# Performance work log

Hardware: AMD Instinct MI355X
Metric: run time of the kernel (lower is better)

Reference implementation:

```python
import jax, jax.numpy as jnp
import numpy as np

NUM_HEADS = 8  # config.num_heads


def setup_inputs() -> dict:
    key = jax.random.key(0)
    k0, k1, k2, k3, k4 = jax.random.split(key, 5)
    B, N, C, E = 32, 20000, 8, 512
    query_embeddings = jax.random.normal(k0, (B, E), dtype=jnp.float32)
    all_embeddings = jax.random.normal(k1, (N, E), dtype=jnp.float32)
    label_mask = jax.random.bernoulli(k2, 0.5, (N, C))  # bool multi-label mask
    # per-class MultiheadAttention q/k in-projection params (torch Linear convention: x @ W.T + b)
    Wq = jax.random.normal(k3, (C, E, E), dtype=jnp.float32) * 0.02
    Wk = jax.random.normal(k4, (C, E, E), dtype=jnp.float32) * 0.02
    bq = jnp.zeros((C, E), dtype=jnp.float32)
    bk = jnp.zeros((C, E), dtype=jnp.float32)
    return {
        "query_embeddings": query_embeddings,
        "all_embeddings": all_embeddings,
        "label_mask": label_mask,
        "Wq": Wq,
        "bq": bq,
        "Wk": Wk,
        "bk": bk,
        "n_samples": 5,
    }


def reference(query_embeddings, all_embeddings, label_mask, Wq, bq, Wk, bk, n_samples):
    """Vectorized-over-classes version of EmbeddingSelector.get_similar_samples.

    For each class c: q = query @ Wq[c].T + bq[c]; k_c over the class's database
    members; per-head scaled-dot softmax; attn weights averaged over heads
    (torch MHA need_weights default); top-k over class members. Non-members are
    masked to -inf before softmax, so they get weight 0 and (since every class
    has >> n_samples members) never enter the top-k -- identical math to the
    per-class gather loop, with global indices returned directly.
    """
    C, E, _ = Wq.shape
    H = NUM_HEADS
    dh = E // H
    B = query_embeddings.shape[0]
    N = all_embeddings.shape[0]

    # per-class projections (torch Linear: x @ W.T + b)
    q = jnp.einsum('be,cfe->cbf', query_embeddings, Wq) + bq[:, None, :]   # (C,B,E)
    k = jnp.einsum('ne,cfe->cnf', all_embeddings, Wk) + bk[:, None, :]     # (C,N,E)
    q = q.reshape(C, B, H, dh)
    k = k.reshape(C, N, H, dh)

    scale = 1.0 / jnp.sqrt(jnp.asarray(dh, q.dtype))
    scores = jnp.einsum('cbhd,cnhd->cbhn', q, k) * scale                   # (C,B,H,N)
    member = jnp.transpose(label_mask)[:, None, None, :]                   # (C,1,1,N)
    scores = jnp.where(member, scores, jnp.asarray(-1e9, scores.dtype))
    attn = jax.nn.softmax(scores, axis=-1).mean(axis=2)                    # (C,B,N) head-avg

    weights, indices = jax.lax.top_k(attn, n_samples)                      # (C,B,ns)
    result_weights = jnp.transpose(weights, (1, 0, 2))                     # (B,C,ns)
    result_indices = jnp.transpose(indices, (1, 0, 2)).astype(jnp.int32)   # (B,C,ns) global ids
    return result_indices, result_weights
```

## Files before the change

kernel.cpp:

```cpp
#include <hip/hip_runtime.h>
#include <math.h>

#define B_  32
#define N_  20000
#define C_  8
#define E_  512
#define H_  8
#define SCALE 0.125f
#define UNSC  9.765625e-4f

#define CHUNK 1024
#define NCH   20
#define NC3   157
#define NCG   20
#define SSZ ((size_t)B_ * H_ * N_)

typedef __attribute__((ext_vector_type(8))) _Float16 h8_t;
typedef __attribute__((ext_vector_type(8))) short   s8_t;
typedef __attribute__((ext_vector_type(4))) float f32x4;

#define MFMAH(a, b, c) __builtin_amdgcn_mfma_f32_16x16x32_f16(a, b, c, 0, 0, 0)

#define GLOAD_LDS16(g, l)                                              \
    __builtin_amdgcn_global_load_lds(                                  \
        (const __attribute__((address_space(1))) unsigned int*)(g),    \
        (__attribute__((address_space(3))) unsigned int*)(l), 16, 0, 0)

__device__ inline unsigned short f16_round(float x, float& fv) {
    _Float16 h = (_Float16)x;
    fv = (float)h;
    union { _Float16 hh; unsigned short us; } u;
    u.hh = h;
    return u.us;
}

__global__ __launch_bounds__(256) void k_q2(
        const float* __restrict__ x, const float* __restrict__ Wq,
        const float* __restrict__ bq, float* __restrict__ q) {
    int ft = blockIdx.x, c = blockIdx.y;
    int f0 = ft * 8;
    __shared__ float wsm[8][66];
    __shared__ float xs[32][66];
    int tid = threadIdx.x;
    int b = tid & 31, fs = tid >> 5;
    float acc = 0.f;
    const float* W = Wq + (size_t)c * E_ * E_;
    for (int k0 = 0; k0 < E_; k0 += 64) {
        __syncthreads();
        for (int i = tid; i < 512; i += 256)
            wsm[i >> 6][i & 63] = W[(size_t)(f0 + (i >> 6)) * E_ + k0 + (i & 63)];
        for (int i = tid; i < 2048; i += 256)
            xs[i >> 6][i & 63] = x[(size_t)(i >> 6) * E_ + k0 + (i & 63)];
        __syncthreads();
        #pragma unroll
        for (int kk = 0; kk < 64; ++kk)
            acc += xs[b][kk] * wsm[fs][kk];
    }
    q[((size_t)c * B_ + b) * E_ + f0 + fs] = acc + bq[c * E_ + f0 + fs];
}

__global__ __launch_bounds__(256) void k_u2(
        const float* __restrict__ q, const float* __restrict__ Wk,
        const float* __restrict__ bk, float* __restrict__ u,
        float* __restrict__ qb) {
    int et = blockIdx.x, h = blockIdx.y, c = blockIdx.z;
    int e0 = et * 64;
    __shared__ float qs[32][66];
    __shared__ float wk[64][66];
    int tid = threadIdx.x;
    int b = tid & 31, es = tid >> 5;
    for (int i = tid; i < 2048; i += 256)
        qs[i >> 6][i & 63] = q[((size_t)c * B_ + (i >> 6)) * E_ + h * 64 + (i & 63)];
    const float* W = Wk + (size_t)c * E_ * E_ + (size_t)(h * 64) * E_;
    for (int i = tid; i < 4096; i += 256)
        wk[i >> 6][i & 63] = W[(size_t)(i >> 6) * E_ + e0 + (i & 63)];
    __syncthreads();
    float acc[8] = {};
    for (int d = 0; d < 64; ++d) {
        float qv = qs[b][d];
        #pragma unroll
        for (int j = 0; j < 8; ++j)
            acc[j] += qv * wk[d][es * 8 + j];
    }
    float* urow = u + ((size_t)c * 256 + b * 8 + h) * E_ + e0 + es * 8;
    #pragma unroll
    for (int j = 0; j < 8; ++j) urow[j] = acc[j];
    if (et == 0 && es == 0) {
        float s = 0.f;
        const float* bkr = bk + c * E_ + h * 64;
        for (int d = 0; d < 64; ++d) s += qs[b][d] * bkr[d];
        qb[c * 256 + b * 8 + h] = s;
    }
}

#define U2P ((size_t)C_ * 16 * 16 * 512)

__global__ void k_split_u2(const float* __restrict__ u, short* __restrict__ u2) {
    int bx = blockIdx.x;
    int ks = bx & 15, mt = (bx >> 4) & 15, c = bx >> 8;
    int lane = threadIdx.x;
    int m  = mt * 16 + (lane & 15);
    int k0 = ks * 32 + (lane >> 4) * 8;
    const float* up = u + ((size_t)c * 256 + m) * 512 + k0;
    size_t base = ((((size_t)c * 16 + mt) * 16 + ks) * 512) + (size_t)lane * 8;
    s8_t vh, vm;
    #pragma unroll
    for (int j = 0; j < 8; ++j) {
        float x = up[j] * 32.0f, fh, fm;
        vh[j] = (short)f16_round(x, fh);
        vm[j] = (short)f16_round(x - fh, fm);
    }
    *(s8_t*)(u2 + base)       = vh;
    *(s8_t*)(u2 + U2P + base) = vm;
}

__global__ void k_split_A2(const float* __restrict__ A, short* __restrict__ A2t) {
    int nc = blockIdx.x, ks = blockIdx.y;
    int tid = threadIdx.x;
    int n = tid >> 1, kg = (tid & 1) * 2;
    int gn = nc * 128 + n;
    const float* ap = A + (size_t)gn * 512 + ks * 32 + kg * 8;
    s8_t vh[2], vm[2];
    #pragma unroll
    for (int g = 0; g < 2; ++g)
        #pragma unroll
        for (int j = 0; j < 8; ++j) {
            float x = (gn < N_) ? ap[g * 8 + j] * 32.0f : 0.f;
            float fh, fm;
            vh[g][j] = (short)f16_round(x, fh);
            vm[g][j] = (short)f16_round(x - fh, fm);
        }
    short* outp = A2t + ((size_t)nc * 16 + ks) * 8192 + n * 32;
    #pragma unroll
    for (int g = 0; g < 2; ++g) {
        int p = ((kg + g) + (n >> 1)) & 3;
        *(s8_t*)(outp + p * 8)        = vh[g];
        *(s8_t*)(outp + 4096 + p * 8) = vm[g];
    }
}

__global__ __launch_bounds__(256, 2) void k_scores_mfma(
        const short* __restrict__ u2, const short* __restrict__ A2t,
        const float* __restrict__ qb, const int* __restrict__ mask,
        float* __restrict__ S, float* __restrict__ Zpart, int c0, int CB) {
    __shared__ __align__(16) short As[16384];
    __shared__ float sQb[256];
    __shared__ int   sMask[128];
    int bx = blockIdx.x;
    int x    = bx & 7;
    int rest = bx >> 3;
    int z    = rest % CB;
    int g    = rest / CB;
    int nc   = g * 8 + x;
    if (nc >= NC3) return;
    int c  = c0 + z;
    int tid = threadIdx.x;
    int lane = tid & 63, w = tid >> 6;
    int quad = lane >> 4, l15 = lane & 15;
    int n0 = nc * 128;

    sQb[tid] = qb[c * 256 + tid];
    if (tid < 128) {
        int n = n0 + tid;
        sMask[tid] = (n < N_) ? mask[(size_t)n * C_ + c] : 0;
    }

    f32x4 acc[4][8];
    #pragma unroll
    for (int i = 0; i < 4; ++i)
        #pragma unroll
        for (int j = 0; j < 8; ++j)
            acc[i][j] = (f32x4){0.f, 0.f, 0.f, 0.f};

    const char* tb = (const char*)A2t + (size_t)nc * 262144;

    for (int ks2 = 0; ks2 < 8; ++ks2) {
        __syncthreads();
        const char* src = tb + (size_t)ks2 * 32768;
        #pragma unroll
        for (int t = 0; t < 8; ++t) {
            int seg = w * 8 + t;
            GLOAD_LDS16(src + (size_t)seg * 1024 + lane * 16,
                        (char*)As + seg * 1024);
        }
        __syncthreads();

        #pragma unroll
        for (int kh = 0; kh < 2; ++kh) {
            int ks = ks2 * 2 + kh;
            const short* Ab = As + kh * 8192;
            h8_t af[4][2];
            #pragma unroll
            for (int mt = 0; mt < 4; ++mt) {
                size_t ub = ((((size_t)c * 16 + (w * 4 + mt)) * 16 + ks) * 512)
                            + (size_t)lane * 8;
                af[mt][0] = *(const h8_t*)(u2 + ub);
                af[mt][1] = *(const h8_t*)(u2 + U2P + ub);
            }
            #pragma unroll
            for (int nt = 0; nt < 8; ++nt) {
                int r = nt * 16 + l15;
                const short* bp = Ab + r * 32 + ((quad + (r >> 1)) & 3) * 8;
                h8_t b0 = *(const h8_t*)bp;
                h8_t b1 = *(const h8_t*)(bp + 4096);
                #pragma unroll
                for (int mt = 0; mt < 4; ++mt) {
                    f32x4 a = acc[mt][nt];
                    a = MFMAH(af[mt][0], b0, a);
                    a = MFMAH(af[mt][0], b1, a);
                    a = MFMAH(af[mt][1], b0, a);
                    acc[mt][nt] = a;
                }
            }
        }
    }

    float* Sc = S + (size_t)z * SSZ;
    #pragma unroll
    for (int mt = 0; mt < 4; ++mt) {
        float rs[4] = {0.f, 0.f, 0.f, 0.f};
        #pragma unroll
        for (int nt = 0; nt < 8; ++nt) {
            int nl = nt * 16 + l15;
            int n = n0 + nl;
            int mem = sMask[nl];
            #pragma unroll
            for (int r = 0; r < 4; ++r) {
                int m = w * 64 + mt * 16 + quad * 4 + r;
                float sc = SCALE * (acc[mt][nt][r] * UNSC + sQb[m]);
                float ev = mem ? __expf(sc) : 0.f;
                rs[r] += ev;
                if (n < N_) Sc[(size_t)m * N_ + n] = ev;
            }
        }
        #pragma unroll
        for (int r = 0; r < 4; ++r) {
            float v = rs[r];
            v += __shfl_xor(v, 1); v += __shfl_xor(v, 2);
            v += __shfl_xor(v, 4); v += __shfl_xor(v, 8);
            if (l15 == 0) {
                int m = w * 64 + mt * 16 + quad * 4 + r;
                Zpart[((size_t)nc * C_ + c) * 256 + m] = v;
            }
        }
    }
}

__global__ void k_zsum(const float* __restrict__ Zpart, float* __restrict__ Z, int c0) {
    int c = c0 + blockIdx.x;
    int i = c * 256 + threadIdx.x;
    float s = 0.f;
    for (int nc = 0; nc < NC3; ++nc) s += Zpart[(size_t)nc * (C_ * 256) + i];
    Z[i] = s;
}

__global__ __launch_bounds__(256) void k_topk1(
        const float* __restrict__ S, const float* __restrict__ Z,
        float2* __restrict__ cand, int c0, int ns) {
    int chunk = blockIdx.x, b = blockIdx.y, z = blockIdx.z;
    const float* Sc = S + (size_t)z * SSZ;
    int tid = threadIdx.x;
    __shared__ float zr[H_];
    if (tid < H_) zr[tid] = 1.0f / Z[(c0 + z) * (B_ * H_) + b * H_ + tid];
    __syncthreads();
    int n0 = chunk * CHUNK + tid * 4;
    bool valid = n0 < N_;
    float4 a = make_float4(0.f, 0.f, 0.f, 0.f);
    if (valid) {
        #pragma unroll
        for (int h = 0; h < H_; ++h) {
            const float4 sv = *(const float4*)&Sc[(size_t)(b * H_ + h) * N_ + n0];
            float wz = zr[h];
            a.x += sv.x * wz; a.y += sv.y * wz; a.z += sv.z * wz; a.w += sv.w * wz;
        }
    }
    float v[4]; int ix[4];
    v[0] = valid ? a.x * 0.125f : -1.f;
    v[1] = valid ? a.y * 0.125f : -1.f;
    v[2] = valid ? a.z * 0.125f : -1.f;
    v[3] = valid ? a.w * 0.125f : -1.f;
    #pragma unroll
    for (int t = 0; t < 4; ++t) ix[t] = valid ? n0 + t : N_;

    __shared__ float wv[4];
    __shared__ int   wi[4];
    __shared__ int   winS;
    int lane = tid & 63, w = tid >> 6;
    for (int j = 0; j < ns; ++j) {
        float bv = v[0]; int bi = ix[0];
        #pragma unroll
        for (int t = 1; t < 4; ++t)
            if (v[t] > bv || (v[t] == bv && ix[t] < bi)) { bv = v[t]; bi = ix[t]; }
        #pragma unroll
        for (int off = 1; off < 64; off <<= 1) {
            float ov = __shfl_xor(bv, off, 64);
            int   oi = __shfl_xor(bi, off, 64);
            if (ov > bv || (ov == bv && oi < bi)) { bv = ov; bi = oi; }
        }
        if (lane == 0) { wv[w] = bv; wi[w] = bi; }
        __syncthreads();
        if (tid == 0) {
            float fv = wv[0]; int fi = wi[0];
            #pragma unroll
            for (int t = 1; t < 4; ++t)
                if (wv[t] > fv || (wv[t] == fv && wi[t] < fi)) { fv = wv[t]; fi = wi[t]; }
            cand[(((size_t)z * B_ + b) * NCH + chunk) * ns + j] =
                make_float2(fv, (float)fi);
            winS = fi;
        }
        __syncthreads();
        int wn = winS;
        #pragma unroll
        for (int t = 0; t < 4; ++t)
            if (ix[t] == wn) v[t] = -2.f;
    }
}

__global__ __launch_bounds__(256) void k_topk2(
        const float2* __restrict__ cand, float* __restrict__ out, int c0, int ns) {
    int b = blockIdx.x, z = blockIdx.y;
    int c = c0 + z;
    int tid = threadIdx.x;
    int ncand = NCH * ns;
    const float2* cb = cand + ((size_t)z * B_ + b) * ncand;
    float v = -3.f; int ix = N_ + 1;
    if (tid < ncand) { float2 e = cb[tid]; v = e.x; ix = (int)e.y; }
    __shared__ float sv[256];
    __shared__ int   si[256];
    __shared__ int   win;
    for (int j = 0; j < ns; ++j) {
        sv[tid] = v; si[tid] = ix;
        __syncthreads();
        for (int w = 128; w >= 1; w >>= 1) {
            if (tid < w) {
                float v2 = sv[tid + w]; int i2 = si[tid + w];
                if (v2 > sv[tid] || (v2 == sv[tid] && i2 < si[tid])) {
                    sv[tid] = v2; si[tid] = i2;
                }
            }
            __syncthreads();
        }
        if (tid == 0) {
            out[((size_t)b * C_ + c) * ns + j] = (float)si[0];
            out[(size_t)B_ * C_ * ns + ((size_t)b * C_ + c) * ns + j] = sv[0];
            win = si[0];
        }
        __syncthreads();
        if (ix == win) v = -3.f;
        __syncthreads();
    }
}

extern "C" void kernel_launch(void* const* d_in, const int* in_sizes, int n_in,
                              void* d_out, int out_size, void* d_ws, size_t ws_size,
                              hipStream_t stream) {
    const float* x    = (const float*)d_in[0];
    const float* A    = (const float*)d_in[1];
    const int*   mask = (const int*)  d_in[2];
    const float* Wq   = (const float*)d_in[3];
    const float* bq   = (const float*)d_in[4];
    const float* Wk   = (const float*)d_in[5];
    const float* bk   = (const float*)d_in[6];
    float* out = (float*)d_out;

    int ns = out_size / (2 * B_ * C_);

    float* ws = (float*)d_ws;
    float* q     = ws;
    float* u     = q     + (size_t)C_ * B_ * E_;
    float* qb    = u     + (size_t)C_ * B_ * H_ * E_;
    float* Z     = qb    + (size_t)C_ * B_ * H_;
    float* Zpart = Z     + (size_t)C_ * B_ * H_;
    short* u2    = (short*)(Zpart + (size_t)NC3 * C_ * 256);
    short* A2t   = u2 + 2 * U2P;
    float* S     = (float*)(A2t + (size_t)NC3 * 16 * 8192);
    size_t fixedFloats = (size_t)(S - ws);

    size_t candFloats = (size_t)C_ * B_ * NCH * ns * 2;
    int CB = 8;
    while (CB > 1 &&
           (fixedFloats + (size_t)CB * SSZ + candFloats + 16) * 4 > ws_size)
        CB >>= 1;
    float2* cand = (float2*)(S + (size_t)CB * SSZ);

    k_q2<<<dim3(64, C_), 256, 0, stream>>>(x, Wq, bq, q);
    k_u2<<<dim3(8, H_, C_), 256, 0, stream>>>(q, Wk, bk, u, qb);
    k_split_u2<<<C_ * 16 * 16, 64, 0, stream>>>(u, u2);
    k_split_A2<<<dim3(NC3, 16), 256, 0, stream>>>(A, A2t);

    for (int c0 = 0; c0 < C_; c0 += CB) {
        k_scores_mfma<<<NCG * 8 * CB, 256, 0, stream>>>(u2, A2t, qb, mask, S, Zpart, c0, CB);
        k_zsum<<<CB, 256, 0, stream>>>(Zpart, Z, c0);
        k_topk1<<<dim3(NCH, B_, CB), 256, 0, stream>>>(S, Z, cand, c0, ns);
        k_topk2<<<dim3(B_, CB), 256, 0, stream>>>(cand, out, c0, ns);
    }
}
```

Measured before the change: 391.8 us.

## Double-buffer LDS tiles in score MFMA kernel to overlap loads with compute

Doubles the shared-memory A tile buffer and prefetches the next k-slab via global_load_lds while the current slab feeds the MFMAs, removing one barrier per iteration. It also raises wave priority around the MFMA bursts with s_setprio and pins instruction order with sched_barrier. LDS use per block doubles to about 64KB, which may lower occupancy below the two blocks per CU requested in launch_bounds.

```diff
diff --git a/kernel.cpp b/kernel.cpp
--- a/kernel.cpp
+++ b/kernel.cpp
@@ -143,7 +143,7 @@
         const short* __restrict__ u2, const short* __restrict__ A2t,
         const float* __restrict__ qb, const int* __restrict__ mask,
         float* __restrict__ S, float* __restrict__ Zpart, int c0, int CB) {
-    __shared__ __align__(16) short As[16384];
+    __shared__ __align__(16) short As[32768];
     __shared__ float sQb[256];
     __shared__ int   sMask[128];
     int bx = blockIdx.x;
@@ -174,45 +174,74 @@
 
     const char* tb = (const char*)A2t + (size_t)nc * 262144;
 
-    for (int ks2 = 0; ks2 < 8; ++ks2) {
-        __syncthreads();
-        const char* src = tb + (size_t)ks2 * 32768;
-        #pragma unroll
-        for (int t = 0; t < 8; ++t) {
-            int seg = w * 8 + t;
-            GLOAD_LDS16(src + (size_t)seg * 1024 + lane * 16,
-                        (char*)As + seg * 1024);
-        }
-        __syncthreads();
-
-        #pragma unroll
-        for (int kh = 0; kh < 2; ++kh) {
-            int ks = ks2 * 2 + kh;
-            const short* Ab = As + kh * 8192;
-            h8_t af[4][2];
+    auto compute_kh = [&](const short* Ab, h8_t (&af)[4][2]) {
+        #pragma unroll
+        for (int nt = 0; nt < 8; ++nt) {
+            int r = nt * 16 + l15;
+            const short* bp = Ab + r * 32 + ((quad + (r >> 1)) & 3) * 8;
+            h8_t b0 = *(const h8_t*)bp;
+            h8_t b1 = *(const h8_t*)(bp + 4096);
+            __builtin_amdgcn_s_setprio(1);
             #pragma unroll
             for (int mt = 0; mt < 4; ++mt) {
-                size_t ub = ((((size_t)c * 16 + (w * 4 + mt)) * 16 + ks) * 512)
-                            + (size_t)lane * 8;
-                af[mt][0] = *(const h8_t*)(u2 + ub);
-                af[mt][1] = *(const h8_t*)(u2 + U2P + ub);
+                f32x4 a = acc[mt][nt];
+                a = MFMAH(af[mt][0], b0, a);
+                a = MFMAH(af[mt][0], b1, a);
+                a = MFMAH(af[mt][1], b0, a);
+                acc[mt][nt] = a;
             }
+            __builtin_amdgcn_s_setprio(0);
+        }
+    };
+
+    #pragma unroll
+    for (int t = 0; t < 8; ++t) {
+        int seg = w * 8 + t;
+        GLOAD_LDS16(tb + (size_t)seg * 1024 + lane * 16,
+                    (char*)As + seg * 1024);
+    }
+    __syncthreads();
+
+    for (int ks2 = 0; ks2 < 8; ++ks2) {
+        const short* Abuf = As + (ks2 & 1) * 16384;
+
+        int ks0 = ks2 * 2;
+        h8_t af0[4][2];
+        #pragma unroll
+        for (int mt = 0; mt < 4; ++mt) {
+            size_t ub = ((((size_t)c * 16 + (w * 4 + mt)) * 16 + ks0) * 512)
+                        + (size_t)lane * 8;
+            af0[mt][0] = *(const h8_t*)(u2 + ub);
+            af0[mt][1] = *(const h8_t*)(u2 + U2P + ub);
+        }
+        __builtin_amdgcn_sched_barrier(0);
+
+        if (ks2 < 7) {
+            const char* src = tb + (size_t)(ks2 + 1) * 32768;
+            char* dst = (char*)As + ((ks2 + 1) & 1) * 32768;
             #pragma unroll
-            for (int nt = 0; nt < 8; ++nt) {
-                int r = nt * 16 + l15;
-                const short* bp = Ab + r * 32 + ((quad + (r >> 1)) & 3) * 8;
-                h8_t b0 = *(const h8_t*)bp;
-                h8_t b1 = *(const h8_t*)(bp + 4096);
-                #pragma unroll
-                for (int mt = 0; mt < 4; ++mt) {
-                    f32x4 a = acc[mt][nt];
-                    a = MFMAH(af[mt][0], b0, a);
-                    a = MFMAH(af[mt][0], b1, a);
-                    a = MFMAH(af[mt][1], b0, a);
-                    acc[mt][nt] = a;
-                }
+            for (int t = 0; t < 8; ++t) {
+                int seg = w * 8 + t;
+                GLOAD_LDS16(src + (size_t)seg * 1024 + lane * 16,
+                            dst + seg * 1024);
             }
         }
+        __builtin_amdgcn_sched_barrier(0);
+
+        compute_kh(Abuf, af0);
+
+        int ks1 = ks0 + 1;
+        h8_t af1[4][2];
+        #pragma unroll
+        for (int mt = 0; mt < 4; ++mt) {
+            size_t ub = ((((size_t)c * 16 + (w * 4 + mt)) * 16 + ks1) * 512)
+                        + (size_t)lane * 8;
+            af1[mt][0] = *(const h8_t*)(u2 + ub);
+            af1[mt][1] = *(const h8_t*)(u2 + U2P + ub);
+        }
+        compute_kh(Abuf + 8192, af1);
+
+        __syncthreads();
     }
 
     float* Sc = S + (size_t)z * SSZ;
```

Result: slower. 406.6 us (+3.8%).

## Split score tile M dimension across two blocks to raise occupancy

Applied to the files above, without the earlier changes.

Each score block now computes only half of the 256 query-head rows, selected by a new mh index. This halves the accumulator and A-fragment registers so the launch bound rises to three blocks per CU, and the grid doubles. It also adds scheduling barriers that split the n-tile loop into halves. The cost is that every 128-column tile of A2t is now staged into LDS twice, doubling that global and LDS traffic.

```diff
diff --git a/kernel.cpp b/kernel.cpp
--- a/kernel.cpp
+++ b/kernel.cpp
@@ -139,19 +139,21 @@
     }
 }
 
-__global__ __launch_bounds__(256, 2) void k_scores_mfma(
+__global__ __launch_bounds__(256, 3) void k_scores_mfma(
         const short* __restrict__ u2, const short* __restrict__ A2t,
         const float* __restrict__ qb, const int* __restrict__ mask,
         float* __restrict__ S, float* __restrict__ Zpart, int c0, int CB) {
     __shared__ __align__(16) short As[16384];
-    __shared__ float sQb[256];
+    __shared__ float sQb[128];
     __shared__ int   sMask[128];
     int bx = blockIdx.x;
-    int x    = bx & 7;
-    int rest = bx >> 3;
-    int z    = rest % CB;
-    int g    = rest / CB;
-    int nc   = g * 8 + x;
+    int x     = bx & 7;
+    int rest  = bx >> 3;
+    int mh    = rest & 1;
+    int rest2 = rest >> 1;
+    int z     = rest2 % CB;
+    int g     = rest2 / CB;
+    int nc    = g * 8 + x;
     if (nc >= NC3) return;
     int c  = c0 + z;
     int tid = threadIdx.x;
@@ -159,15 +161,15 @@
     int quad = lane >> 4, l15 = lane & 15;
     int n0 = nc * 128;
 
-    sQb[tid] = qb[c * 256 + tid];
     if (tid < 128) {
+        sQb[tid] = qb[c * 256 + mh * 128 + tid];
         int n = n0 + tid;
         sMask[tid] = (n < N_) ? mask[(size_t)n * C_ + c] : 0;
     }
 
-    f32x4 acc[4][8];
-    #pragma unroll
-    for (int i = 0; i < 4; ++i)
+    f32x4 acc[2][8];
+    #pragma unroll
+    for (int i = 0; i < 2; ++i)
         #pragma unroll
         for (int j = 0; j < 8; ++j)
             acc[i][j] = (f32x4){0.f, 0.f, 0.f, 0.f};
@@ -189,27 +191,33 @@
         for (int kh = 0; kh < 2; ++kh) {
             int ks = ks2 * 2 + kh;
             const short* Ab = As + kh * 8192;
-            h8_t af[4][2];
+            h8_t af[2][2];
             #pragma unroll
-            for (int mt = 0; mt < 4; ++mt) {
-                size_t ub = ((((size_t)c * 16 + (w * 4 + mt)) * 16 + ks) * 512)
+            for (int mt = 0; mt < 2; ++mt) {
+                int mtg = mh * 8 + w * 2 + mt;
+                size_t ub = ((((size_t)c * 16 + mtg) * 16 + ks) * 512)
                             + (size_t)lane * 8;
                 af[mt][0] = *(const h8_t*)(u2 + ub);
                 af[mt][1] = *(const h8_t*)(u2 + U2P + ub);
             }
             #pragma unroll
-            for (int nt = 0; nt < 8; ++nt) {
-                int r = nt * 16 + l15;
-                const short* bp = Ab + r * 32 + ((quad + (r >> 1)) & 3) * 8;
-                h8_t b0 = *(const h8_t*)bp;
-                h8_t b1 = *(const h8_t*)(bp + 4096);
+            for (int half = 0; half < 2; ++half) {
+                __builtin_amdgcn_sched_barrier(0);
                 #pragma unroll
-                for (int mt = 0; mt < 4; ++mt) {
-                    f32x4 a = acc[mt][nt];
-                    a = MFMAH(af[mt][0], b0, a);
-                    a = MFMAH(af[mt][0], b1, a);
-                    a = MFMAH(af[mt][1], b0, a);
-                    acc[mt][nt] = a;
+                for (int q4 = 0; q4 < 4; ++q4) {
+                    int nt = half * 4 + q4;
+                    int r = nt * 16 + l15;
+                    const short* bp = Ab + r * 32 + ((quad + (r >> 1)) & 3) * 8;
+                    h8_t b0 = *(const h8_t*)bp;
+                    h8_t b1 = *(const h8_t*)(bp + 4096);
+                    #pragma unroll
+                    for (int mt = 0; mt < 2; ++mt) {
+                        f32x4 a = acc[mt][nt];
+                        a = MFMAH(af[mt][0], b0, a);
+                        a = MFMAH(af[mt][0], b1, a);
+                        a = MFMAH(af[mt][1], b0, a);
+                        acc[mt][nt] = a;
+                    }
                 }
             }
         }
@@ -217,7 +225,7 @@
 
     float* Sc = S + (size_t)z * SSZ;
     #pragma unroll
-    for (int mt = 0; mt < 4; ++mt) {
+    for (int mt = 0; mt < 2; ++mt) {
         float rs[4] = {0.f, 0.f, 0.f, 0.f};
         #pragma unroll
         for (int nt = 0; nt < 8; ++nt) {
@@ -226,11 +234,11 @@
             int mem = sMask[nl];
             #pragma unroll
             for (int r = 0; r < 4; ++r) {
-                int m = w * 64 + mt * 16 + quad * 4 + r;
-                float sc = SCALE * (acc[mt][nt][r] * UNSC + sQb[m]);
+                int ml = w * 32 + mt * 16 + quad * 4 + r;
+                float sc = SCALE * (acc[mt][nt][r] * UNSC + sQb[ml]);
                 float ev = mem ? __expf(sc) : 0.f;
                 rs[r] += ev;
-                if (n < N_) Sc[(size_t)m * N_ + n] = ev;
+                if (n < N_) Sc[(size_t)(mh * 128 + ml) * N_ + n] = ev;
             }
         }
         #pragma unroll
@@ -239,8 +247,8 @@
             v += __shfl_xor(v, 1); v += __shfl_xor(v, 2);
             v += __shfl_xor(v, 4); v += __shfl_xor(v, 8);
             if (l15 == 0) {
-                int m = w * 64 + mt * 16 + quad * 4 + r;
-                Zpart[((size_t)nc * C_ + c) * 256 + m] = v;
+                int ml = w * 32 + mt * 16 + quad * 4 + r;
+                Zpart[((size_t)nc * C_ + c) * 256 + mh * 128 + ml] = v;
             }
         }
     }
@@ -389,7 +397,7 @@
     k_split_A2<<<dim3(NC3, 16), 256, 0, stream>>>(A, A2t);
 
     for (int c0 = 0; c0 < C_; c0 += CB) {
-        k_scores_mfma<<<NCG * 8 * CB, 256, 0, stream>>>(u2, A2t, qb, mask, S, Zpart, c0, CB);
+        k_scores_mfma<<<NCG * 2 * 8 * CB, 256, 0, stream>>>(u2, A2t, qb, mask, S, Zpart, c0, CB);
         k_zsum<<<CB, 256, 0, stream>>>(Zpart, Z, c0);
         k_topk1<<<dim3(NCH, B_, CB), 256, 0, stream>>>(S, Z, cand, c0, ns);
         k_topk2<<<dim3(B_, CB), 256, 0, stream>>>(cand, out, c0, ns);
```

Result: faster. 373.3 us (-4.7%).
